# Kernel tuning notes

Measured on AMD Instinct MI355X. Metric: run time of the kernel, lower is better.

## Reference

```python
import jax, jax.numpy as jnp
import numpy as np

ATT = 128  # attention_size
D = 128    # entity_embedding_dim


def setup_inputs() -> dict:
    key = jax.random.key(0)
    k1, k2, k3, k4, k5 = jax.random.split(key, 5)
    B, N, K = 1024, 50, 5
    entity_embedding = jax.random.normal(k1, (B, N, D), dtype=jnp.float32)
    neigh_entity_embedding = jax.random.normal(k2, (B, N, K, D), dtype=jnp.float32)
    neigh_relation_embedding = jax.random.normal(k3, (B, N, K, D), dtype=jnp.float32)
    # fc1: Linear(3*D -> ATT), fc2: Linear(ATT -> 1)
    lim1 = 1.0 / np.sqrt(3 * D)
    lim2 = 1.0 / np.sqrt(ATT)
    W1 = jax.random.uniform(k4, (3 * D, ATT), minval=-lim1, maxval=lim1, dtype=jnp.float32)
    b1 = jnp.zeros((ATT,), dtype=jnp.float32)
    W2 = jax.random.uniform(k5, (ATT, 1), minval=-lim2, maxval=lim2, dtype=jnp.float32)
    b2 = jnp.zeros((1,), dtype=jnp.float32)
    return {
        "entity_embedding": entity_embedding,
        "neigh_entity_embedding": neigh_entity_embedding,
        "neigh_relation_embedding": neigh_relation_embedding,
        "W1": W1, "b1": b1, "W2": W2, "b2": b2,
    }


def reference(entity_embedding, neigh_entity_embedding, neigh_relation_embedding, W1, b1, W2, b2):
    B, N, K, Dd = neigh_entity_embedding.shape
    # expand entity to each of the K neighbors: [B, N, K, D]
    ent_exp = jnp.broadcast_to(entity_embedding[:, :, None, :], (B, N, K, Dd))
    # concat along feature dim -> [B, N, K, 3D]
    concat = jnp.concatenate([ent_exp, neigh_entity_embedding, neigh_relation_embedding], axis=3)
    # tiny MLP: fc1 -> fc2 gives one logit per neighbor
    h = jnp.einsum('bnkf,fa->bnka', concat, W1) + b1          # [B, N, K, ATT]
    logits = jnp.einsum('bnka,ao->bnko', h, W2) + b2          # [B, N, K, 1]
    att = jax.nn.softmax(logits, axis=2)                      # softmax over K neighbors
    neigh_att = jnp.sum(att * neigh_entity_embedding, axis=2) # [B, N, D]
    # squeeze() on [B,N,D] with no singleton dims is identity
    return jnp.concatenate([entity_embedding, neigh_att], axis=-1)  # [B, N, 2D]
```

## Files before the change

kernel.cpp:

```cpp
#include <hip/hip_runtime.h>
#include <math.h>


#define DIM 128
#define KN 5

typedef float nfloat4 __attribute__((ext_vector_type(4)));

__device__ __forceinline__ float dot4(nfloat4 a, nfloat4 b) {
    return a.x * b.x + a.y * b.y + a.z * b.z + a.w * b.w;
}

template <int CTRL>
__device__ __forceinline__ float dpp_add(float v) {
    int x = __builtin_amdgcn_update_dpp(0, __float_as_int(v), CTRL, 0xF, 0xF, true);
    return v + __int_as_float(x);
}

__device__ __forceinline__ float half_reduce(float v) {
    v = dpp_add<0xB1>(v);
    v = dpp_add<0x4E>(v);
    v = dpp_add<0x124>(v);
    v = dpp_add<0x128>(v);
    v += __int_as_float(__builtin_amdgcn_ds_swizzle(__float_as_int(v), 0x401F));
    return v;
}

__global__ __launch_bounds__(256) void kgat_prep(
    const float* __restrict__ W1,
    const float* __restrict__ W2,
    float* __restrict__ ws)
{
    const int t = blockIdx.x * 4 + (threadIdx.x >> 6);
    const int lane = threadIdx.x & 63;
    if (t < 2 * DIM) {
        const float2 w1 = *(const float2*)(W1 + (size_t)(DIM + t) * DIM + 2 * lane);
        const float2 w2 = *(const float2*)(W2 + 2 * lane);
        float v = w1.x * w2.x + w1.y * w2.y;
        #pragma unroll
        for (int off = 32; off >= 1; off >>= 1) v += __shfl_xor(v, off, 64);
        if (lane == 0) ws[t] = v;
    }
}

__global__ __launch_bounds__(256) void kgat_main(
    const float* __restrict__ ent,
    const float* __restrict__ ne,
    const float* __restrict__ nr,
    const float* __restrict__ ws,
    float* __restrict__ out,
    int P)
{
    const int wave = threadIdx.x >> 6;
    const int lane = threadIdx.x & 63;
    const int half = lane >> 5;
    const int l    = lane & 31;
    const int p = blockIdx.x * 8 + wave * 2 + half;
    if (p >= P) return;

    const int d = l * 4;
    const nfloat4 wne = *(const nfloat4*)(ws + d);
    const nfloat4 wnr = *(const nfloat4*)(ws + DIM + d);

    const nfloat4 e4 = *(const nfloat4*)(ent + (size_t)p * DIM + d);
    const size_t rowK = ((size_t)p * KN) * DIM + d;
    nfloat4 ne4[KN], nr4[KN];
    #pragma unroll
    for (int k = 0; k < KN; ++k) {
        ne4[k] = *(const nfloat4*)(ne + rowK + (size_t)k * DIM);
        nr4[k] = *(const nfloat4*)(nr + rowK + (size_t)k * DIM);
    }

    float logit[KN];
    #pragma unroll
    for (int k = 0; k < KN; ++k)
        logit[k] = half_reduce(dot4(ne4[k], wne) + dot4(nr4[k], wnr));

    float m = -INFINITY;
    #pragma unroll
    for (int k = 0; k < KN; ++k) m = fmaxf(m, logit[k]);
    float ex[KN], s = 0.f;
    #pragma unroll
    for (int k = 0; k < KN; ++k) { ex[k] = __expf(logit[k] - m); s += ex[k]; }
    const float inv = 1.f / s;

    nfloat4 acc = {0.f, 0.f, 0.f, 0.f};
    #pragma unroll
    for (int k = 0; k < KN; ++k) {
        const float a = ex[k] * inv;
        acc.x += a * ne4[k].x;
        acc.y += a * ne4[k].y;
        acc.z += a * ne4[k].z;
        acc.w += a * ne4[k].w;
    }

    float* orow = out + (size_t)p * (2 * DIM);
    __builtin_nontemporal_store(e4,  (nfloat4*)(orow + d));
    __builtin_nontemporal_store(acc, (nfloat4*)(orow + DIM + d));
}

extern "C" void kernel_launch(void* const* d_in, const int* in_sizes, int n_in,
                              void* d_out, int out_size, void* d_ws, size_t ws_size,
                              hipStream_t stream) {
    const float* ent = (const float*)d_in[0];
    const float* ne  = (const float*)d_in[1];
    const float* nr  = (const float*)d_in[2];
    const float* W1  = (const float*)d_in[3];
    const float* W2  = (const float*)d_in[5];
    float* out = (float*)d_out;
    float* ws  = (float*)d_ws;

    const int P = in_sizes[0] / DIM;

    kgat_prep<<<(2 * DIM + 3) / 4, 256, 0, stream>>>(W1, W2, ws);
    kgat_main<<<(P + 7) / 8, 256, 0, stream>>>(ent, ne, nr, ws, out, P);
}
```

Before: 313.2 us.

## Grid-stride main kernel with double-buffered register prefetch across rows

Each wave now handles ITER row pairs in a grid-stride loop and issues the next row's loads before computing the current one, using two register buffers. The grid shrinks by ITER, which cuts block launch overhead and overlaps memory latency with compute. In exchange it doubles register use for the buffers, which may lower occupancy, and it exposes fewer waves in flight for a purely bandwidth-bound stream.

```diff
diff --git a/kernel.cpp b/kernel.cpp
--- a/kernel.cpp
+++ b/kernel.cpp
@@ -4,6 +4,7 @@
 
 #define DIM 128
 #define KN 5
+#define ITER 4
 
 typedef float nfloat4 __attribute__((ext_vector_type(4)));
 
@@ -55,48 +56,75 @@
     const int lane = threadIdx.x & 63;
     const int half = lane >> 5;
     const int l    = lane & 31;
-    const int p = blockIdx.x * 8 + wave * 2 + half;
-    if (p >= P) return;
+    const int nwaves = gridDim.x * 4;
+    const int gw = blockIdx.x * 4 + wave;
+    const int d = l * 4;
 
-    const int d = l * 4;
     const nfloat4 wne = *(const nfloat4*)(ws + d);
     const nfloat4 wnr = *(const nfloat4*)(ws + DIM + d);
 
-    const nfloat4 e4 = *(const nfloat4*)(ent + (size_t)p * DIM + d);
-    const size_t rowK = ((size_t)p * KN) * DIM + d;
-    nfloat4 ne4[KN], nr4[KN];
-    #pragma unroll
-    for (int k = 0; k < KN; ++k) {
-        ne4[k] = *(const nfloat4*)(ne + rowK + (size_t)k * DIM);
-        nr4[k] = *(const nfloat4*)(nr + rowK + (size_t)k * DIM);
+    nfloat4 e4[2];
+    nfloat4 ne4[2][KN], nr4[2][KN];
+
+    int p = gw * 2 + half;
+    const int stride = nwaves * 2;
+
+    if (p < P) {
+        e4[0] = *(const nfloat4*)(ent + (size_t)p * DIM + d);
+        const size_t rowK = ((size_t)p * KN) * DIM + d;
+        #pragma unroll
+        for (int k = 0; k < KN; ++k) {
+            ne4[0][k] = *(const nfloat4*)(ne + rowK + (size_t)k * DIM);
+            nr4[0][k] = *(const nfloat4*)(nr + rowK + (size_t)k * DIM);
+        }
     }
 
-    float logit[KN];
     #pragma unroll
-    for (int k = 0; k < KN; ++k)
-        logit[k] = half_reduce(dot4(ne4[k], wne) + dot4(nr4[k], wnr));
+    for (int i = 0; i < ITER; ++i) {
+        const int cur = i & 1;
+        const int nxt = cur ^ 1;
+        const int pn = p + stride;
 
-    float m = -INFINITY;
-    #pragma unroll
-    for (int k = 0; k < KN; ++k) m = fmaxf(m, logit[k]);
-    float ex[KN], s = 0.f;
-    #pragma unroll
-    for (int k = 0; k < KN; ++k) { ex[k] = __expf(logit[k] - m); s += ex[k]; }
-    const float inv = 1.f / s;
+        if (i + 1 < ITER && pn < P) {
+            e4[nxt] = *(const nfloat4*)(ent + (size_t)pn * DIM + d);
+            const size_t rowKn = ((size_t)pn * KN) * DIM + d;
+            #pragma unroll
+            for (int k = 0; k < KN; ++k) {
+                ne4[nxt][k] = *(const nfloat4*)(ne + rowKn + (size_t)k * DIM);
+                nr4[nxt][k] = *(const nfloat4*)(nr + rowKn + (size_t)k * DIM);
+            }
+        }
 
-    nfloat4 acc = {0.f, 0.f, 0.f, 0.f};
-    #pragma unroll
-    for (int k = 0; k < KN; ++k) {
-        const float a = ex[k] * inv;
-        acc.x += a * ne4[k].x;
-        acc.y += a * ne4[k].y;
-        acc.z += a * ne4[k].z;
-        acc.w += a * ne4[k].w;
+        if (p < P) {
+            float logit[KN];
+            #pragma unroll
+            for (int k = 0; k < KN; ++k)
+                logit[k] = half_reduce(dot4(ne4[cur][k], wne) + dot4(nr4[cur][k], wnr));
+
+            float m = -INFINITY;
+            #pragma unroll
+            for (int k = 0; k < KN; ++k) m = fmaxf(m, logit[k]);
+            float ex[KN], s = 0.f;
+            #pragma unroll
+            for (int k = 0; k < KN; ++k) { ex[k] = __expf(logit[k] - m); s += ex[k]; }
+            const float inv = 1.f / s;
+
+            nfloat4 acc = {0.f, 0.f, 0.f, 0.f};
+            #pragma unroll
+            for (int k = 0; k < KN; ++k) {
+                const float a = ex[k] * inv;
+                acc.x += a * ne4[cur][k].x;
+                acc.y += a * ne4[cur][k].y;
+                acc.z += a * ne4[cur][k].z;
+                acc.w += a * ne4[cur][k].w;
+            }
+
+            float* orow = out + (size_t)p * (2 * DIM);
+            __builtin_nontemporal_store(e4[cur], (nfloat4*)(orow + d));
+            __builtin_nontemporal_store(acc,     (nfloat4*)(orow + DIM + d));
+        }
+        p = pn;
     }
-
-    float* orow = out + (size_t)p * (2 * DIM);
-    __builtin_nontemporal_store(e4,  (nfloat4*)(orow + d));
-    __builtin_nontemporal_store(acc, (nfloat4*)(orow + DIM + d));
 }
 
 extern "C" void kernel_launch(void* const* d_in, const int* in_sizes, int n_in,
@@ -113,5 +141,6 @@
     const int P = in_sizes[0] / DIM;
 
     kgat_prep<<<(2 * DIM + 3) / 4, 256, 0, stream>>>(W1, W2, ws);
-    kgat_main<<<(P + 7) / 8, 256, 0, stream>>>(ent, ne, nr, ws, out, P);
+    const int blocks = (P + 8 * ITER - 1) / (8 * ITER);
+    kgat_main<<<blocks, 256, 0, stream>>>(ent, ne, nr, ws, out, P);
 }
```

Measured after the change: 317.2 us. No clear change (+1.3%).
